# Performance work log

Measured on AMD Instinct MI355X. Metric: run time of the kernel, lower is better.

Reference implementation:

```python
import jax, jax.numpy as jnp
import numpy as np

H = 16  # num_heads
LN_EPS = 1e-5


def setup_inputs() -> dict:
    key = jax.random.key(0)
    ks = jax.random.split(key, 16)
    B, L, E = 4, 1024, 1024
    x = jax.random.normal(ks[0], (B, L, E), dtype=jnp.float32)
    bias = jax.random.normal(ks[1], (B, H, L, L), dtype=jnp.float32)
    mask = jax.random.randint(ks[2], (B, L), 0, 2, dtype=jnp.int32)
    w = lambda k: jax.random.normal(k, (E, E), dtype=jnp.float32) * 0.02
    return {
        "x": x, "bias": bias, "mask": mask,
        "Wq": w(ks[3]), "bq": jnp.zeros((E,), jnp.float32),
        "Wk": w(ks[4]), "bk": jnp.zeros((E,), jnp.float32),
        "Wv": w(ks[5]), "bv": jnp.zeros((E,), jnp.float32),
        "Wo": w(ks[6]), "bo": jnp.zeros((E,), jnp.float32),
        "gamma": jnp.ones((E,), jnp.float32),
        "beta": jnp.zeros((E,), jnp.float32),
        "gate": jax.random.normal(ks[7], (H,), dtype=jnp.float32) * 0.1,
    }


def reference(x, bias, mask, Wq, bq, Wk, bk, Wv, bv, Wo, bo, gamma, beta, gate):
    B, L, E = x.shape
    D = E // H
    scale = 1.0 / jnp.sqrt(jnp.float32(D))
    residual = x
    # LayerNorm
    mu = jnp.mean(x, axis=-1, keepdims=True)
    var = jnp.mean(jnp.square(x - mu), axis=-1, keepdims=True)
    xn = (x - mu) * jax.lax.rsqrt(var + LN_EPS) * gamma + beta

    def proj(W, b):  # [B,L,E] -> [B,H,L,D]
        return (xn @ W.T + b).reshape(B, L, H, D).transpose(0, 2, 1, 3)

    Q, K, V = proj(Wq, bq), proj(Wk, bk), proj(Wv, bv)
    # logits = QK^T/sqrt(D) + alpha_h * bias   -> [B,H,L,L]
    logits = jnp.einsum("bhqd,bhkd->bhqk", Q, K) * scale
    logits = logits + gate[None, :, None, None] * bias
    mf = mask.astype(x.dtype)
    logits = logits + (1.0 - mf)[:, None, None, :] * -10000.0  # key mask
    attn = jax.nn.softmax(logits, axis=-1)
    attn = jnp.nan_to_num(attn) * mf[:, None, :, None]  # query mask
    out = jnp.einsum("bhqk,bhkd->bqhd", attn, V).reshape(B, L, E)
    out = out * mf[..., None]
    return residual + out @ Wo.T + bo
```

## Files before the change

kernel.cpp:

```cpp
#include <hip/hip_runtime.h>
#include <math.h>

typedef unsigned short u16;
typedef __attribute__((ext_vector_type(8))) short bf16x8;
typedef __attribute__((ext_vector_type(4))) float f32x4;

#define MFMA16(a, b, c) __builtin_amdgcn_mfma_f32_16x16x32_bf16(a, b, c, 0, 0, 0)

__device__ __forceinline__ void gld16(const void* g, void* l) {
  __builtin_amdgcn_global_load_lds((const __attribute__((address_space(1))) void*)g,
                                   (__attribute__((address_space(3))) void*)l, 16, 0, 0);
}

__device__ __forceinline__ u16 f2bf(float f) {
  unsigned u = __float_as_uint(f);
  u += 0x7fffu + ((u >> 16) & 1u);
  return (u16)(u >> 16);
}

__global__ __launch_bounds__(256) void k_castw(const float* __restrict__ wq, const float* __restrict__ wk,
                                               const float* __restrict__ wv, const float* __restrict__ wo,
                                               u16* __restrict__ dst) {
  int t = blockIdx.x * 256 + threadIdx.x;
  int which = t >> 18;
  int off = (t & 0x3ffff) << 2;
  const float* src = (which == 0) ? wq : (which == 1) ? wk : (which == 2) ? wv : wo;
  float4 v = *reinterpret_cast<const float4*>(src + off);
  ushort4 o;
  o.x = f2bf(v.x); o.y = f2bf(v.y); o.z = f2bf(v.z); o.w = f2bf(v.w);
  *reinterpret_cast<ushort4*>(dst + ((size_t)which << 20) + off) = o;
}

__global__ __launch_bounds__(256) void k_ln(const float* __restrict__ x, const float* __restrict__ gamma,
                                            const float* __restrict__ beta, u16* __restrict__ xn) {
  const int row = blockIdx.x, tid = threadIdx.x;
  const int lane = tid & 63, w = tid >> 6;
  const float* xr = x + (size_t)row * 1024;
  float4 v = *reinterpret_cast<const float4*>(xr + tid * 4);
  float s = v.x + v.y + v.z + v.w;
  float s2 = v.x * v.x + v.y * v.y + v.z * v.z + v.w * v.w;
  #pragma unroll
  for (int m = 1; m < 64; m <<= 1) { s += __shfl_xor(s, m); s2 += __shfl_xor(s2, m); }
  __shared__ float ps[4], pq[4];
  if (lane == 0) { ps[w] = s; pq[w] = s2; }
  __syncthreads();
  float S = ps[0] + ps[1] + ps[2] + ps[3];
  float S2 = pq[0] + pq[1] + pq[2] + pq[3];
  float mu = S * (1.f / 1024.f);
  float var = S2 * (1.f / 1024.f) - mu * mu;
  float rstd = rsqrtf(var + 1e-5f);
  float4 g = *reinterpret_cast<const float4*>(gamma + tid * 4);
  float4 bt = *reinterpret_cast<const float4*>(beta + tid * 4);
  ushort4 o;
  o.x = f2bf((v.x - mu) * rstd * g.x + bt.x);
  o.y = f2bf((v.y - mu) * rstd * g.y + bt.y);
  o.z = f2bf((v.z - mu) * rstd * g.z + bt.z);
  o.w = f2bf((v.w - mu) * rstd * g.w + bt.w);
  *reinterpret_cast<ushort4*>(xn + (size_t)row * 1024 + tid * 4) = o;
}

__global__ __launch_bounds__(256) void k_gemm_qkv(const u16* __restrict__ xn,
    const u16* __restrict__ wqb, const u16* __restrict__ wkb, const u16* __restrict__ wvb,
    const float* __restrict__ bq, const float* __restrict__ bk, const float* __restrict__ bv,
    u16* __restrict__ qo, u16* __restrict__ ko, u16* __restrict__ vo) {
  __shared__ __align__(16) u16 lA[128 * 32];
  __shared__ __align__(16) u16 lB[128 * 32];
  const int tid = threadIdx.x;
  const int w = tid >> 6, lane = tid & 63;
  const int wr = w >> 1, wc = w & 1;
  const int lane15 = lane & 15, lgrp = lane >> 4;
  const int m0 = blockIdx.y * 128, n0 = blockIdx.x * 128;
  const int z = blockIdx.z;
  const u16* Bt = (z == 0) ? wqb : (z == 1) ? wkb : wvb;

  f32x4 zero = {0.f, 0.f, 0.f, 0.f};
  f32x4 acc[4][4];
  #pragma unroll
  for (int i = 0; i < 4; i++)
    #pragma unroll
    for (int j = 0; j < 4; j++) acc[i][j] = zero;

  const int srow = w * 16 + (lane >> 2);
  const int scol = (lane & 3) * 8;
  for (int kt = 0; kt < 32; kt++) {
    const int k0 = kt * 32;
    #pragma unroll
    for (int c = 0; c < 2; c++) {
      gld16(xn + (size_t)(m0 + c * 64 + srow) * 1024 + k0 + scol, (char*)lA + c * 4096 + w * 1024);
      gld16(Bt + (size_t)(n0 + c * 64 + srow) * 1024 + k0 + scol, (char*)lB + c * 4096 + w * 1024);
    }
    __syncthreads();
    bf16x8 aF[4], bF[4];
    #pragma unroll
    for (int f = 0; f < 4; f++) {
      aF[f] = *reinterpret_cast<const bf16x8*>(&lA[(wr * 64 + f * 16 + lane15) * 32 + lgrp * 8]);
      bF[f] = *reinterpret_cast<const bf16x8*>(&lB[(wc * 64 + f * 16 + lane15) * 32 + lgrp * 8]);
    }
    #pragma unroll
    for (int fm = 0; fm < 4; fm++)
      #pragma unroll
      for (int fn = 0; fn < 4; fn++)
        acc[fm][fn] = MFMA16(aF[fm], bF[fn], acc[fm][fn]);
    __syncthreads();
  }

  const float* bvec = (z == 0) ? bq : (z == 1) ? bk : bv;
  u16* dst = (z == 0) ? qo : (z == 1) ? ko : vo;
  #pragma unroll
  for (int fm = 0; fm < 4; fm++)
    #pragma unroll
    for (int fn = 0; fn < 4; fn++) {
      const int n = n0 + wc * 64 + fn * 16 + lane15;
      const int h = n >> 6, d = n & 63;
      const float bn = bvec[n];
      #pragma unroll
      for (int j = 0; j < 4; j++) {
        const int m = m0 + wr * 64 + fm * 16 + lgrp * 4 + j;
        const int b = m >> 10, lq = m & 1023;
        dst[(((size_t)(b * 16 + h)) * 1024 + lq) * 64 + d] = f2bf(acc[fm][fn][j] + bn);
      }
    }
}

__global__ __launch_bounds__(256) void k_transpose_v(const u16* __restrict__ V, u16* __restrict__ Vt) {
  __shared__ u16 t[64][64];
  const int bh = blockIdx.y, l0 = blockIdx.x * 64;
  const int tid = threadIdx.x;
  const int r = tid >> 2, c0 = (tid & 3) * 16;
  const u16* src = V + ((size_t)bh * 1024 + l0 + r) * 64 + c0;
  __align__(16) u16 tmp[16];
  *reinterpret_cast<uint4*>(tmp) = *reinterpret_cast<const uint4*>(src);
  *reinterpret_cast<uint4*>(tmp + 8) = *reinterpret_cast<const uint4*>(src + 8);
  #pragma unroll
  for (int i = 0; i < 16; i++) t[c0 + i][r] = tmp[i];
  __syncthreads();
  __align__(16) u16 o[16];
  #pragma unroll
  for (int i = 0; i < 16; i++) o[i] = t[r][c0 + i];
  u16* dst = Vt + ((size_t)bh * 64 + r) * 1024 + l0 + c0;
  *reinterpret_cast<uint4*>(dst) = *reinterpret_cast<const uint4*>(o);
  *reinterpret_cast<uint4*>(dst + 8) = *reinterpret_cast<const uint4*>(o + 8);
}

__global__ __launch_bounds__(256) void k_attn(const u16* __restrict__ Q, const u16* __restrict__ K,
    const u16* __restrict__ Vt, const float* __restrict__ bias, const int* __restrict__ mask,
    const float* __restrict__ gate, u16* __restrict__ O) {
  __shared__ __align__(16) u16 lK[2][4096];
  __shared__ __align__(16) u16 lV[2][4096];
  __shared__ __align__(16) u16 lP[4][16 * 72];
  const int tid = threadIdx.x;
  const int w = tid >> 6, lane = tid & 63;
  const int l15 = lane & 15, lg4 = lane >> 4;
  const int bh = blockIdx.y;
  const int b = bh >> 4, h = bh & 15;
  const int qg = blockIdx.x * 64 + w * 16 + l15;
  const float gateh = gate[h];
  const int* mb = mask + b * 1024;
  const float* biasr = bias + ((size_t)bh << 20) + (size_t)qg * 1024;
  const size_t kvbase = (size_t)bh * 65536;

  bf16x8 qf0 = *reinterpret_cast<const bf16x8*>(Q + kvbase + (size_t)qg * 64 + lg4 * 8);
  bf16x8 qf1 = *reinterpret_cast<const bf16x8*>(Q + kvbase + (size_t)qg * 64 + 32 + lg4 * 8);

  f32x4 zero = {0.f, 0.f, 0.f, 0.f};
  float m_i = -INFINITY, l_i = 0.f;
  f32x4 accO[4];
  #pragma unroll
  for (int f = 0; f < 4; f++) accO[f] = zero;

  const int srow = w * 8 + (lane >> 3);
  const int scol = ((lane & 7) ^ (lane >> 3)) * 8;
  const int ldst = w * 1024;
  const int swz = (l15 & 7) << 4;

  #pragma unroll
  for (int c = 0; c < 2; c++) {
    gld16(K + kvbase + (size_t)(c * 32 + srow) * 64 + scol, (char*)lK[0] + c * 4096 + ldst);
    gld16(Vt + kvbase + (size_t)(c * 32 + srow) * 1024 + scol, (char*)lV[0] + c * 4096 + ldst);
  }
  __syncthreads();

  int cur = 0;
  for (int t = 0; t < 16; t++) {
    const int kb = t * 64;
    if (t < 15) {
      const int kb2 = kb + 64;
      #pragma unroll
      for (int c = 0; c < 2; c++) {
        gld16(K + kvbase + (size_t)(kb2 + c * 32 + srow) * 64 + scol, (char*)lK[cur ^ 1] + c * 4096 + ldst);
        gld16(Vt + kvbase + (size_t)(c * 32 + srow) * 1024 + kb2 + scol, (char*)lV[cur ^ 1] + c * 4096 + ldst);
      }
    }

    const char* lkb = (const char*)lK[cur];
    f32x4 s[4];
    #pragma unroll
    for (int fn = 0; fn < 4; fn++) {
      const char* rowp = lkb + (fn * 16 + l15) * 128;
      bf16x8 kf0 = *reinterpret_cast<const bf16x8*>(rowp + ((lg4 * 16) ^ swz));
      bf16x8 kf1 = *reinterpret_cast<const bf16x8*>(rowp + ((64 + lg4 * 16) ^ swz));
      s[fn] = MFMA16(kf0, qf0, zero);
      s[fn] = MFMA16(kf1, qf1, s[fn]);
    }

    float p[16];
    float pmax = -INFINITY;
    #pragma unroll
    for (int fn = 0; fn < 4; fn++) {
      const int kg = kb + fn * 16 + lg4 * 4;
      float4 b4 = *reinterpret_cast<const float4*>(biasr + kg);
      int4 m4 = *reinterpret_cast<const int4*>(mb + kg);
      #pragma unroll
      for (int j = 0; j < 4; j++) {
        const float bj = (j == 0) ? b4.x : (j == 1) ? b4.y : (j == 2) ? b4.z : b4.w;
        const int mj = (j == 0) ? m4.x : (j == 1) ? m4.y : (j == 2) ? m4.z : m4.w;
        float lgt = s[fn][j] * 0.125f + gateh * bj + (mj ? 0.f : -10000.f);
        p[fn * 4 + j] = lgt;
        pmax = fmaxf(pmax, lgt);
      }
    }
    pmax = fmaxf(pmax, __shfl_xor(pmax, 16));
    pmax = fmaxf(pmax, __shfl_xor(pmax, 32));
    const float mnew = fmaxf(m_i, pmax);
    const float corr = __expf(m_i - mnew);
    float rs = 0.f;
    #pragma unroll
    for (int i = 0; i < 16; i++) { p[i] = __expf(p[i] - mnew); rs += p[i]; }
    rs += __shfl_xor(rs, 16);
    rs += __shfl_xor(rs, 32);
    l_i = l_i * corr + rs;
    m_i = mnew;
    #pragma unroll
    for (int f = 0; f < 4; f++)
      #pragma unroll
      for (int j = 0; j < 4; j++) accO[f][j] *= corr;

    u16* lpw = lP[w];
    #pragma unroll
    for (int fn = 0; fn < 4; fn++) {
      ushort4 pk;
      pk.x = f2bf(p[fn * 4 + 0]); pk.y = f2bf(p[fn * 4 + 1]);
      pk.z = f2bf(p[fn * 4 + 2]); pk.w = f2bf(p[fn * 4 + 3]);
      *reinterpret_cast<ushort4*>(lpw + l15 * 72 + fn * 16 + lg4 * 4) = pk;
    }

    bf16x8 pf0 = *reinterpret_cast<const bf16x8*>((const char*)lpw + l15 * 144 + lg4 * 16);
    bf16x8 pf1 = *reinterpret_cast<const bf16x8*>((const char*)lpw + l15 * 144 + 64 + lg4 * 16);
    const char* lvb = (const char*)lV[cur];
    #pragma unroll
    for (int f = 0; f < 4; f++) {
      const char* rowp = lvb + (f * 16 + l15) * 128;
      bf16x8 vf0 = *reinterpret_cast<const bf16x8*>(rowp + ((lg4 * 16) ^ swz));
      bf16x8 vf1 = *reinterpret_cast<const bf16x8*>(rowp + ((64 + lg4 * 16) ^ swz));
      accO[f] = MFMA16(vf0, pf0, accO[f]);
      accO[f] = MFMA16(vf1, pf1, accO[f]);
    }
    __syncthreads();
    cur ^= 1;
  }

  const float sc = (mb[qg] ? 1.f : 0.f) / l_i;
  u16* orow = O + (((size_t)(b * 1024 + qg)) * 16 + h) * 64;
  #pragma unroll
  for (int f = 0; f < 4; f++) {
    ushort4 o4;
    o4.x = f2bf(accO[f][0] * sc); o4.y = f2bf(accO[f][1] * sc);
    o4.z = f2bf(accO[f][2] * sc); o4.w = f2bf(accO[f][3] * sc);
    *reinterpret_cast<ushort4*>(orow + f * 16 + lg4 * 4) = o4;
  }
}

__global__ __launch_bounds__(256) void k_gemm_out(const u16* __restrict__ A, const u16* __restrict__ Bt,
    const float* __restrict__ bo, const float* __restrict__ x, float* __restrict__ out) {
  __shared__ __align__(16) u16 lA[128 * 32];
  __shared__ __align__(16) u16 lB[128 * 32];
  const int tid = threadIdx.x;
  const int w = tid >> 6, lane = tid & 63;
  const int wr = w >> 1, wc = w & 1;
  const int lane15 = lane & 15, lgrp = lane >> 4;
  const int m0 = blockIdx.y * 128, n0 = blockIdx.x * 128;

  f32x4 zero = {0.f, 0.f, 0.f, 0.f};
  f32x4 acc[4][4];
  #pragma unroll
  for (int i = 0; i < 4; i++)
    #pragma unroll
    for (int j = 0; j < 4; j++) acc[i][j] = zero;

  const int srow = w * 16 + (lane >> 2);
  const int scol = (lane & 3) * 8;
  for (int kt = 0; kt < 32; kt++) {
    const int k0 = kt * 32;
    #pragma unroll
    for (int c = 0; c < 2; c++) {
      gld16(A + (size_t)(m0 + c * 64 + srow) * 1024 + k0 + scol, (char*)lA + c * 4096 + w * 1024);
      gld16(Bt + (size_t)(n0 + c * 64 + srow) * 1024 + k0 + scol, (char*)lB + c * 4096 + w * 1024);
    }
    __syncthreads();
    bf16x8 aF[4], bF[4];
    #pragma unroll
    for (int f = 0; f < 4; f++) {
      aF[f] = *reinterpret_cast<const bf16x8*>(&lA[(wr * 64 + f * 16 + lane15) * 32 + lgrp * 8]);
      bF[f] = *reinterpret_cast<const bf16x8*>(&lB[(wc * 64 + f * 16 + lane15) * 32 + lgrp * 8]);
    }
    #pragma unroll
    for (int fm = 0; fm < 4; fm++)
      #pragma unroll
      for (int fn = 0; fn < 4; fn++)
        acc[fm][fn] = MFMA16(aF[fm], bF[fn], acc[fm][fn]);
    __syncthreads();
  }

  #pragma unroll
  for (int fm = 0; fm < 4; fm++)
    #pragma unroll
    for (int fn = 0; fn < 4; fn++) {
      const int n = n0 + wc * 64 + fn * 16 + lane15;
      const float bn = bo[n];
      #pragma unroll
      for (int j = 0; j < 4; j++) {
        const int m = m0 + wr * 64 + fm * 16 + lgrp * 4 + j;
        out[(size_t)m * 1024 + n] = acc[fm][fn][j] + bn + x[(size_t)m * 1024 + n];
      }
    }
}

extern "C" void kernel_launch(void* const* d_in, const int* in_sizes, int n_in,
                              void* d_out, int out_size, void* d_ws, size_t ws_size,
                              hipStream_t stream) {
  const float* x     = (const float*)d_in[0];
  const float* bias  = (const float*)d_in[1];
  const int*   mask  = (const int*)d_in[2];
  const float* Wq    = (const float*)d_in[3];
  const float* bq    = (const float*)d_in[4];
  const float* Wk    = (const float*)d_in[5];
  const float* bk    = (const float*)d_in[6];
  const float* Wv    = (const float*)d_in[7];
  const float* bv    = (const float*)d_in[8];
  const float* Wo    = (const float*)d_in[9];
  const float* bo    = (const float*)d_in[10];
  const float* gamma = (const float*)d_in[11];
  const float* beta  = (const float*)d_in[12];
  const float* gate  = (const float*)d_in[13];
  float* out = (float*)d_out;

  u16* wsu  = (u16*)d_ws;
  u16* wqb  = wsu;
  u16* wkb  = wqb  + (1u << 20);
  u16* wvb  = wkb  + (1u << 20);
  u16* wob  = wvb  + (1u << 20);
  u16* xnb  = wob  + (1u << 20);
  u16* qb   = xnb  + (4u << 20);
  u16* kbuf = qb   + (4u << 20);
  u16* vb   = kbuf + (4u << 20);
  u16* vtb  = vb   + (4u << 20);
  u16* ob   = vtb  + (4u << 20);

  k_castw<<<4096, 256, 0, stream>>>(Wq, Wk, Wv, Wo, wqb);
  k_ln<<<4096, 256, 0, stream>>>(x, gamma, beta, xnb);
  k_gemm_qkv<<<dim3(8, 32, 3), 256, 0, stream>>>(xnb, wqb, wkb, wvb, bq, bk, bv, qb, kbuf, vb);
  k_transpose_v<<<dim3(16, 64), 256, 0, stream>>>(vb, vtb);
  k_attn<<<dim3(16, 64), 256, 0, stream>>>(qb, kbuf, vtb, bias, mask, gate, ob);
  k_gemm_out<<<dim3(8, 32), 256, 0, stream>>>(ob, wob, bo, x, out);
}
```

Measured before the change: 542.0 us.

## Prefetch bias/mask one tile ahead, fold softmax scale into Q, swizzle P buffer

The attention kernel now loads the next tile's bias and mask one iteration ahead into registers, combined with gate and mask offset, so the global bias read overlaps with the current tile's MFMA and softmax work. The 1/sqrt(D) scale is moved into the Q projection epilogue, removing a multiply per logit. The P staging buffer in LDS switches from padded rows to an XOR-swizzled layout, and launch bounds request 4 blocks per CU. The register prefetch raises register pressure, which could conflict with the occupancy hint, and scaling Q before bf16 rounding slightly changes numerics.

Measured after the change: 511.5 us. 5.6% less time.

```diff
diff --git a/kernel.cpp b/kernel.cpp
--- a/kernel.cpp
+++ b/kernel.cpp
@@ -106,6 +106,7 @@
 
   const float* bvec = (z == 0) ? bq : (z == 1) ? bk : bv;
   u16* dst = (z == 0) ? qo : (z == 1) ? ko : vo;
+  const float oscale = (z == 0) ? 0.125f : 1.0f;
   #pragma unroll
   for (int fm = 0; fm < 4; fm++)
     #pragma unroll
@@ -117,7 +118,7 @@
       for (int j = 0; j < 4; j++) {
         const int m = m0 + wr * 64 + fm * 16 + lgrp * 4 + j;
         const int b = m >> 10, lq = m & 1023;
-        dst[(((size_t)(b * 16 + h)) * 1024 + lq) * 64 + d] = f2bf(acc[fm][fn][j] + bn);
+        dst[(((size_t)(b * 16 + h)) * 1024 + lq) * 64 + d] = f2bf((acc[fm][fn][j] + bn) * oscale);
       }
     }
 }
@@ -142,12 +143,12 @@
   *reinterpret_cast<uint4*>(dst + 8) = *reinterpret_cast<const uint4*>(o + 8);
 }
 
-__global__ __launch_bounds__(256) void k_attn(const u16* __restrict__ Q, const u16* __restrict__ K,
+__global__ __launch_bounds__(256, 4) void k_attn(const u16* __restrict__ Q, const u16* __restrict__ K,
     const u16* __restrict__ Vt, const float* __restrict__ bias, const int* __restrict__ mask,
     const float* __restrict__ gate, u16* __restrict__ O) {
   __shared__ __align__(16) u16 lK[2][4096];
   __shared__ __align__(16) u16 lV[2][4096];
-  __shared__ __align__(16) u16 lP[4][16 * 72];
+  __shared__ __align__(16) u16 lP[4][1024];
   const int tid = threadIdx.x;
   const int w = tid >> 6, lane = tid & 63;
   const int l15 = lane & 15, lg4 = lane >> 4;
@@ -178,17 +179,38 @@
     gld16(K + kvbase + (size_t)(c * 32 + srow) * 64 + scol, (char*)lK[0] + c * 4096 + ldst);
     gld16(Vt + kvbase + (size_t)(c * 32 + srow) * 1024 + scol, (char*)lV[0] + c * 4096 + ldst);
   }
+  f32x4 bcur[4];
+  #pragma unroll
+  for (int fn = 0; fn < 4; fn++) {
+    const int kg = fn * 16 + lg4 * 4;
+    float4 b4 = *reinterpret_cast<const float4*>(biasr + kg);
+    int4 m4 = *reinterpret_cast<const int4*>(mb + kg);
+    bcur[fn][0] = gateh * b4.x + (m4.x ? 0.f : -10000.f);
+    bcur[fn][1] = gateh * b4.y + (m4.y ? 0.f : -10000.f);
+    bcur[fn][2] = gateh * b4.z + (m4.z ? 0.f : -10000.f);
+    bcur[fn][3] = gateh * b4.w + (m4.w ? 0.f : -10000.f);
+  }
   __syncthreads();
 
   int cur = 0;
   for (int t = 0; t < 16; t++) {
-    const int kb = t * 64;
+    f32x4 bnext[4];
     if (t < 15) {
-      const int kb2 = kb + 64;
+      const int kb2 = (t + 1) * 64;
       #pragma unroll
       for (int c = 0; c < 2; c++) {
         gld16(K + kvbase + (size_t)(kb2 + c * 32 + srow) * 64 + scol, (char*)lK[cur ^ 1] + c * 4096 + ldst);
         gld16(Vt + kvbase + (size_t)(c * 32 + srow) * 1024 + kb2 + scol, (char*)lV[cur ^ 1] + c * 4096 + ldst);
+      }
+      #pragma unroll
+      for (int fn = 0; fn < 4; fn++) {
+        const int kg = kb2 + fn * 16 + lg4 * 4;
+        float4 b4 = *reinterpret_cast<const float4*>(biasr + kg);
+        int4 m4 = *reinterpret_cast<const int4*>(mb + kg);
+        bnext[fn][0] = gateh * b4.x + (m4.x ? 0.f : -10000.f);
+        bnext[fn][1] = gateh * b4.y + (m4.y ? 0.f : -10000.f);
+        bnext[fn][2] = gateh * b4.z + (m4.z ? 0.f : -10000.f);
+        bnext[fn][3] = gateh * b4.w + (m4.w ? 0.f : -10000.f);
       }
     }
 
@@ -206,19 +228,13 @@
     float p[16];
     float pmax = -INFINITY;
     #pragma unroll
-    for (int fn = 0; fn < 4; fn++) {
-      const int kg = kb + fn * 16 + lg4 * 4;
-      float4 b4 = *reinterpret_cast<const float4*>(biasr + kg);
-      int4 m4 = *reinterpret_cast<const int4*>(mb + kg);
+    for (int fn = 0; fn < 4; fn++)
       #pragma unroll
       for (int j = 0; j < 4; j++) {
-        const float bj = (j == 0) ? b4.x : (j == 1) ? b4.y : (j == 2) ? b4.z : b4.w;
-        const int mj = (j == 0) ? m4.x : (j == 1) ? m4.y : (j == 2) ? m4.z : m4.w;
-        float lgt = s[fn][j] * 0.125f + gateh * bj + (mj ? 0.f : -10000.f);
+        float lgt = s[fn][j] + bcur[fn][j];
         p[fn * 4 + j] = lgt;
         pmax = fmaxf(pmax, lgt);
       }
-    }
     pmax = fmaxf(pmax, __shfl_xor(pmax, 16));
     pmax = fmaxf(pmax, __shfl_xor(pmax, 32));
     const float mnew = fmaxf(m_i, pmax);
@@ -235,17 +251,17 @@
       #pragma unroll
       for (int j = 0; j < 4; j++) accO[f][j] *= corr;
 
-    u16* lpw = lP[w];
+    char* lpw = (char*)lP[w];
     #pragma unroll
     for (int fn = 0; fn < 4; fn++) {
       ushort4 pk;
       pk.x = f2bf(p[fn * 4 + 0]); pk.y = f2bf(p[fn * 4 + 1]);
       pk.z = f2bf(p[fn * 4 + 2]); pk.w = f2bf(p[fn * 4 + 3]);
-      *reinterpret_cast<ushort4*>(lpw + l15 * 72 + fn * 16 + lg4 * 4) = pk;
-    }
-
-    bf16x8 pf0 = *reinterpret_cast<const bf16x8*>((const char*)lpw + l15 * 144 + lg4 * 16);
-    bf16x8 pf1 = *reinterpret_cast<const bf16x8*>((const char*)lpw + l15 * 144 + 64 + lg4 * 16);
+      *reinterpret_cast<ushort4*>(lpw + ((l15 * 128 + fn * 32 + lg4 * 8) ^ swz)) = pk;
+    }
+
+    bf16x8 pf0 = *reinterpret_cast<const bf16x8*>(lpw + ((l15 * 128 + lg4 * 16) ^ swz));
+    bf16x8 pf1 = *reinterpret_cast<const bf16x8*>(lpw + ((l15 * 128 + 64 + lg4 * 16) ^ swz));
     const char* lvb = (const char*)lV[cur];
     #pragma unroll
     for (int f = 0; f < 4; f++) {
@@ -256,6 +272,10 @@
       accO[f] = MFMA16(vf1, pf1, accO[f]);
     }
     __syncthreads();
+    if (t < 15) {
+      #pragma unroll
+      for (int fn = 0; fn < 4; fn++) bcur[fn] = bnext[fn];
+    }
     cur ^= 1;
   }
 
```
